# Kernel tuning notes

Hardware: AMD Instinct MI355X
Metric: run time of the kernel (lower is better)

## Reference

```python
import jax, jax.numpy as jnp
import numpy as np
import math

NEIGHBOR_RADIUS = 30.0

def _masked_softmax(logits, mask, axis):
    # mask: bool, True = keep; all-masked rows return zeros
    p = jax.nn.softmax(jnp.where(mask, logits, -1e9), axis=axis) * mask.astype(logits.dtype)
    return p / jnp.clip(jnp.sum(p, axis=axis, keepdims=True), 1e-9, None)

def _forward(agents_state, agents_mask, map_polylines, map_poly_mask,
             map_poly_type, map_tl_status, map_on_route,
             pm_w1, pm_b1, pm_w2, pm_b2, type_emb, tl_emb, route_emb,
             mo_w1, mo_b1, mo_w2, mo_b2,
             ae_w1, ae_b1, ae_w2, ae_b2, ae_w3, ae_b3,
             mr_w1, mr_b1, mr_w2, mr_b2,
             nr_w1, nr_b1, nr_w2, nr_b2,
             to_w1, to_b1, to_w2, to_b2):
    relu = jax.nn.relu
    a_mask = (agents_mask > 0.5).astype(agents_state.dtype)   # (B,N,T)
    a_feat = agents_state[..., :5]
    # ---- map polyline node encoder ----
    h = relu(map_polylines @ pm_w1 + pm_b1)                   # (B,M,L,H)
    h = relu(h @ pm_w2 + pm_b2)
    h = h.max(axis=2)                                         # (B,M,H) max-pool over points
    t_idx = jnp.clip(map_poly_type, 0, type_emb.shape[0] - 1)
    s_idx = jnp.clip(map_tl_status, 0, tl_emb.shape[0] - 1)
    r_idx = jnp.clip(map_on_route, 0, route_emb.shape[0] - 1)
    h = h + type_emb[t_idx] + tl_emb[s_idx] + route_emb[r_idx]
    h = relu(h @ mo_w1 + mo_b1) @ mo_w2 + mo_b2
    map_mask = map_poly_mask > 0.5                            # (B,M) bool
    map_node = h * map_mask[..., None].astype(h.dtype)        # (B,M,D)
    map_center = map_polylines.mean(axis=2)                   # (B,M,2)
    # ---- agent state encoder ----
    a = relu(a_feat @ ae_w1 + ae_b1)
    a = relu(a @ ae_w2 + ae_b2)
    a_emb = (a @ ae_w3 + ae_b3) * a_mask[..., None]           # (B,N,T,D)
    D = a_emb.shape[-1]
    # ---- agent -> map attention ----
    agent_pos = a_feat[..., 0:2]
    rel = map_center[:, None, None, :, :] - agent_pos[:, :, :, None, :]  # (B,N,T,M,2)
    dist = jnp.linalg.norm(rel, axis=-1, keepdims=True)
    rel_feat = jnp.concatenate([rel, dist], axis=-1)          # (B,N,T,M,3)
    rel_score = (relu(rel_feat @ mr_w1 + mr_b1) @ mr_w2 + mr_b2)[..., 0]  # (B,N,T,M)
    dot = jnp.einsum('bntd,bmd->bntm', a_emb, map_node) / math.sqrt(D)
    score_mask = jnp.broadcast_to(map_mask[:, None, None, :], dot.shape)
    attn = _masked_softmax(dot + rel_score, score_mask, axis=-1)
    map_ctx = jnp.einsum('bntm,bmd->bntd', attn, map_node)    # (B,N,T,D)
    # ---- neighbor graph attention ----
    pos = a_feat[..., 0:2]
    vel = a_feat[..., 3:5]
    pos_j = jnp.transpose(pos, (0, 2, 1, 3))                  # (B,T,N,2)
    vel_j = jnp.transpose(vel, (0, 2, 1, 3))
    rel_pos = pos_j[:, None, :, :, :] - pos[:, :, :, None, :] # (B,N,T,N,2) = p_j - p_i
    rel_vel = vel_j[:, None, :, :, :] - vel[:, :, :, None, :]
    dist_ij = jnp.linalg.norm(rel_pos, axis=-1, keepdims=True)
    rel_ij = jnp.concatenate([rel_pos, rel_vel, dist_ij], axis=-1)        # (B,N,T,N,5)
    nbr_score = (relu(rel_ij @ nr_w1 + nr_b1) @ nr_w2 + nr_b2)[..., 0]    # (B,N,T,N)
    am_b = agents_mask > 0.5
    valid_i = am_b[..., None]                                 # (B,N,T,1)
    valid_j = jnp.transpose(am_b, (0, 2, 1))[:, None, :, :]   # (B,1,T,N)
    N = pos.shape[1]
    not_self = ~jnp.eye(N, dtype=bool)[None, :, None, :]      # (1,N,1,N)
    nbr_mask = valid_i & valid_j & (dist_ij[..., 0] <= NEIGHBOR_RADIUS) & not_self
    dot_n = jnp.einsum('bitd,bjtd->bitj', a_emb, a_emb) / math.sqrt(D)
    w_n = _masked_softmax(dot_n + nbr_score, nbr_mask, axis=-1)
    nbr_ctx = jnp.einsum('bitj,bjtd->bitd', w_n, a_emb)       # (B,N,T,D)
    # ---- tau head ----
    tau = jnp.concatenate([a_emb, map_ctx, nbr_ctx], axis=-1)
    tau = relu(tau @ to_w1 + to_b1) @ to_w2 + to_b2
    return tau * a_mask[..., None]

def setup_inputs() -> dict:
    key = jax.random.key(0)
    B, N, T, M, L = 2, 32, 32, 256, 20
    H, D, TAU = 128, 128, 64
    ks = jax.random.split(key, 32)
    def f(i, shp):
        return jax.random.normal(ks[i], shp, jnp.float32) * 0.05
    inp = {}
    inp['agents_state'] = jax.random.normal(ks[0], (B, N, T, 5), jnp.float32) * jnp.array([50., 50., 1., 5., 5.], jnp.float32)
    inp['agents_mask'] = jnp.ones((B, N, T), jnp.float32)
    inp['map_polylines'] = jax.random.normal(ks[1], (B, M, L, 2), jnp.float32) * 50.0
    inp['map_poly_mask'] = jnp.ones((B, M), jnp.float32)
    inp['map_poly_type'] = jax.random.randint(ks[2], (B, M), 0, 4)
    inp['map_tl_status'] = jax.random.randint(ks[3], (B, M), 0, 8)
    inp['map_on_route'] = jax.random.randint(ks[4], (B, M), 0, 2)
    inp['pm_w1'] = f(5, (2, H));  inp['pm_b1'] = jnp.zeros((H,), jnp.float32)
    inp['pm_w2'] = f(6, (H, H)); inp['pm_b2'] = jnp.zeros((H,), jnp.float32)
    inp['type_emb'] = f(7, (4, H)); inp['tl_emb'] = f(8, (8, H)); inp['route_emb'] = f(9, (2, H))
    inp['mo_w1'] = f(10, (H, H)); inp['mo_b1'] = jnp.zeros((H,), jnp.float32)
    inp['mo_w2'] = f(11, (H, D)); inp['mo_b2'] = jnp.zeros((D,), jnp.float32)
    inp['ae_w1'] = f(12, (5, H)); inp['ae_b1'] = jnp.zeros((H,), jnp.float32)
    inp['ae_w2'] = f(13, (H, H)); inp['ae_b2'] = jnp.zeros((H,), jnp.float32)
    inp['ae_w3'] = f(14, (H, D)); inp['ae_b3'] = jnp.zeros((D,), jnp.float32)
    inp['mr_w1'] = f(15, (3, H)); inp['mr_b1'] = jnp.zeros((H,), jnp.float32)
    inp['mr_w2'] = f(16, (H, 1)); inp['mr_b2'] = jnp.zeros((1,), jnp.float32)
    inp['nr_w1'] = f(17, (5, H)); inp['nr_b1'] = jnp.zeros((H,), jnp.float32)
    inp['nr_w2'] = f(18, (H, 1)); inp['nr_b2'] = jnp.zeros((1,), jnp.float32)
    inp['to_w1'] = f(19, (3 * D, H)); inp['to_b1'] = jnp.zeros((H,), jnp.float32)
    inp['to_w2'] = f(20, (H, TAU)); inp['to_b2'] = jnp.zeros((TAU,), jnp.float32)
    return inp

def reference(agents_state, agents_mask, map_polylines, map_poly_mask,
              map_poly_type, map_tl_status, map_on_route,
              pm_w1, pm_b1, pm_w2, pm_b2, type_emb, tl_emb, route_emb,
              mo_w1, mo_b1, mo_w2, mo_b2,
              ae_w1, ae_b1, ae_w2, ae_b2, ae_w3, ae_b3,
              mr_w1, mr_b1, mr_w2, mr_b2,
              nr_w1, nr_b1, nr_w2, nr_b2,
              to_w1, to_b1, to_w2, to_b2):
    return _forward(agents_state, agents_mask, map_polylines, map_poly_mask,
                    map_poly_type, map_tl_status, map_on_route,
                    pm_w1, pm_b1, pm_w2, pm_b2, type_emb, tl_emb, route_emb,
                    mo_w1, mo_b1, mo_w2, mo_b2,
                    ae_w1, ae_b1, ae_w2, ae_b2, ae_w3, ae_b3,
                    mr_w1, mr_b1, mr_w2, mr_b2,
                    nr_w1, nr_b1, nr_w2, nr_b2,
                    to_w1, to_b1, to_w2, to_b2)
```

## Files before the change

kernel.cpp:

```cpp
#include <hip/hip_runtime.h>
#include <hip/hip_bf16.h>

#define Bb 2
#define Nn 32
#define Tt 32
#define Mm 256
#define Ll 20
#define Hh 128
#define Dd 128
#define TAUu 64
#define RSQRT_D 0.08838834764831843f

__global__ __launch_bounds__(256) void k_map(
    const float* __restrict__ poly, const float* __restrict__ pmask,
    const int* __restrict__ ptype, const int* __restrict__ ptl, const int* __restrict__ proute,
    const float* __restrict__ pm_w1, const float* __restrict__ pm_b1,
    const float* __restrict__ pm_w2, const float* __restrict__ pm_b2,
    const float* __restrict__ type_emb, const float* __restrict__ tl_emb, const float* __restrict__ route_emb,
    const float* __restrict__ mo_w1, const float* __restrict__ mo_b1,
    const float* __restrict__ mo_w2, const float* __restrict__ mo_b2,
    float* __restrict__ map_node, float* __restrict__ map_nodeT, float* __restrict__ map_center)
{
    int bm = blockIdx.x;
    int b  = bm >> 8;
    int m  = bm & 255;
    int tid = threadIdx.x;
    int h    = tid & 127;
    int half = tid >> 7;
    __shared__ float pts[Ll*2];
    __shared__ float h1a[Ll][Hh];
    __shared__ float hv[Hh];
    __shared__ float red[Hh];
    if (tid < Ll*2) pts[tid] = poly[bm*Ll*2 + tid];
    __syncthreads();
    float w1x = pm_w1[h];
    float w1y = pm_w1[Hh+h];
    float bb1 = pm_b1[h];
    int l0 = half*10;
    #pragma unroll
    for (int u = 0; u < 10; ++u) {
        int l = l0 + u;
        h1a[l][h] = fmaxf(fmaf(w1x, pts[2*l], fmaf(w1y, pts[2*l+1], bb1)), 0.f);
    }
    __syncthreads();
    float bb2 = pm_b2[h];
    float acc[10];
    #pragma unroll
    for (int u = 0; u < 10; ++u) acc[u] = bb2;
    for (int k = 0; k < Hh; ++k) {
        float w = pm_w2[k*Hh + h];
        #pragma unroll
        for (int u = 0; u < 10; ++u) acc[u] = fmaf(h1a[l0+u][k], w, acc[u]);
    }
    float mx = 0.f;
    #pragma unroll
    for (int u = 0; u < 10; ++u) mx = fmaxf(mx, acc[u]);
    if (half == 1) red[h] = mx;
    __syncthreads();
    if (half == 0) {
        float mm2 = fmaxf(mx, red[h]);
        int ti = min(max(ptype[bm], 0), 3);
        int si = min(max(ptl[bm], 0), 7);
        int ri = min(max(proute[bm], 0), 1);
        hv[h] = mm2 + type_emb[ti*Hh+h] + tl_emb[si*Hh+h] + route_emb[ri*Hh+h];
    }
    __syncthreads();
    float a1 = 0.f;
    for (int k = half*64; k < half*64 + 64; ++k) a1 = fmaf(hv[k], mo_w1[k*Hh+h], a1);
    if (half == 1) red[h] = a1;
    __syncthreads();
    if (half == 0) hv[h] = fmaxf(a1 + red[h] + mo_b1[h], 0.f);
    __syncthreads();
    float a2 = 0.f;
    for (int k = half*64; k < half*64 + 64; ++k) a2 = fmaf(hv[k], mo_w2[k*Dd+h], a2);
    if (half == 1) red[h] = a2;
    __syncthreads();
    if (half == 0) {
        float val = a2 + red[h] + mo_b2[h];
        float mk = (pmask[bm] > 0.5f) ? 1.f : 0.f;
        val *= mk;
        map_node[bm*Dd + h] = val;
        map_nodeT[(b*Dd + h)*Mm + m] = val;
    }
    if (tid == 0) {
        float sx = 0.f, sy = 0.f;
        for (int l = 0; l < Ll; ++l) { sx += pts[2*l]; sy += pts[2*l+1]; }
        map_center[bm*2+0] = sx / (float)Ll;
        map_center[bm*2+1] = sy / (float)Ll;
    }
}

__global__ __launch_bounds__(128) void k_agent(
    const float* __restrict__ astate, const float* __restrict__ amask,
    const float* __restrict__ ae_w1, const float* __restrict__ ae_b1,
    const float* __restrict__ ae_w2, const float* __restrict__ ae_b2,
    const float* __restrict__ ae_w3, const float* __restrict__ ae_b3,
    float* __restrict__ a_emb)
{
    int r0 = blockIdx.x * 4;
    int h  = threadIdx.x;
    __shared__ float f5[4][5];
    __shared__ float a1s[4][Hh];
    if (h < 20) f5[h/5][h%5] = astate[(r0 + h/5)*5 + (h%5)];
    __syncthreads();
    float acc[4];
    float b1v = ae_b1[h];
    #pragma unroll
    for (int r = 0; r < 4; ++r) acc[r] = b1v;
    #pragma unroll
    for (int k = 0; k < 5; ++k) {
        float w = ae_w1[k*Hh + h];
        #pragma unroll
        for (int r = 0; r < 4; ++r) acc[r] = fmaf(f5[r][k], w, acc[r]);
    }
    #pragma unroll
    for (int r = 0; r < 4; ++r) a1s[r][h] = fmaxf(acc[r], 0.f);
    __syncthreads();
    float b2v = ae_b2[h];
    #pragma unroll
    for (int r = 0; r < 4; ++r) acc[r] = b2v;
    for (int k = 0; k < Hh; ++k) {
        float w = ae_w2[k*Hh + h];
        #pragma unroll
        for (int r = 0; r < 4; ++r) acc[r] = fmaf(a1s[r][k], w, acc[r]);
    }
    float v2[4];
    #pragma unroll
    for (int r = 0; r < 4; ++r) v2[r] = fmaxf(acc[r], 0.f);
    __syncthreads();
    #pragma unroll
    for (int r = 0; r < 4; ++r) a1s[r][h] = v2[r];
    __syncthreads();
    float b3v = ae_b3[h];
    #pragma unroll
    for (int r = 0; r < 4; ++r) acc[r] = b3v;
    for (int k = 0; k < Hh; ++k) {
        float w = ae_w3[k*Dd + h];
        #pragma unroll
        for (int r = 0; r < 4; ++r) acc[r] = fmaf(a1s[r][k], w, acc[r]);
    }
    #pragma unroll
    for (int r = 0; r < 4; ++r) {
        float mk = (amask[r0+r] > 0.5f) ? 1.f : 0.f;
        a_emb[(r0+r)*Dd + h] = acc[r] * mk;
    }
}

__global__ __launch_bounds__(256) void k_mapattn(
    const float* __restrict__ astate, const float* __restrict__ pmask,
    const float* __restrict__ a_emb, const float* __restrict__ map_node,
    const float* __restrict__ map_nodeT, const float* __restrict__ map_center,
    const float* __restrict__ mr_w1, const float* __restrict__ mr_b1,
    const float* __restrict__ mr_w2, const float* __restrict__ mr_b2,
    float* __restrict__ map_ctx)
{
    int r0  = blockIdx.x * 4;
    int b   = r0 >> 10;
    int tid = threadIdx.x;
    __shared__ float w1m[3*Hh];
    __shared__ float b1m[Hh];
    __shared__ float w2m[Hh];
    __shared__ float pxy4[4][2];
    __shared__ float ae4[4][Dd];
    __shared__ float lg4[4][Mm];
    __shared__ float redc[4][Dd];
    for (int q = tid; q < 3*Hh; q += 256) w1m[q] = mr_w1[q];
    if (tid < Hh) { b1m[tid] = mr_b1[tid]; w2m[tid] = mr_w2[tid]; }
    for (int q = tid; q < 512; q += 256) ae4[q>>7][q&127] = a_emb[(r0 + (q>>7))*Dd + (q&127)];
    if (tid < 8) pxy4[tid>>1][tid&1] = astate[(r0 + (tid>>1))*5 + (tid&1)];
    float b2c = mr_b2[0];
    __syncthreads();

    {
        int m = tid;
        float cx = map_center[(b*Mm+m)*2+0];
        float cy = map_center[(b*Mm+m)*2+1];
        float rx[4], ry[4], dv[4], sA[4], dt[4];
        #pragma unroll
        for (int r = 0; r < 4; ++r) {
            rx[r] = cx - pxy4[r][0];
            ry[r] = cy - pxy4[r][1];
            dv[r] = sqrtf(rx[r]*rx[r] + ry[r]*ry[r]);
            sA[r] = b2c;
            dt[r] = 0.f;
        }
        for (int hh = 0; hh < Hh; ++hh) {
            float wa = w1m[hh], wb = w1m[Hh+hh], wc = w1m[2*Hh+hh];
            float bbv = b1m[hh], w2v = w2m[hh];
            #pragma unroll
            for (int r = 0; r < 4; ++r) {
                float t1 = fmaxf(fmaf(rx[r], wa, fmaf(ry[r], wb, fmaf(dv[r], wc, bbv))), 0.f);
                sA[r] = fmaf(t1, w2v, sA[r]);
            }
        }
        for (int d = 0; d < Dd; ++d) {
            float v = map_nodeT[(b*Dd + d)*Mm + m];
            #pragma unroll
            for (int r = 0; r < 4; ++r) dt[r] = fmaf(ae4[r][d], v, dt[r]);
        }
        bool mk = pmask[b*Mm+m] > 0.5f;
        #pragma unroll
        for (int r = 0; r < 4; ++r)
            lg4[r][m] = mk ? fmaf(dt[r], RSQRT_D, sA[r]) : -1e30f;
    }
    __syncthreads();

    {
        int w = tid >> 6, lam = tid & 63;
        float x0 = lg4[w][lam], x1 = lg4[w][64+lam], x2 = lg4[w][128+lam], x3 = lg4[w][192+lam];
        float mxv = fmaxf(fmaxf(x0,x1), fmaxf(x2,x3));
        for (int off = 32; off; off >>= 1) mxv = fmaxf(mxv, __shfl_xor(mxv, off));
        float e0 = (x0 > -1e29f) ? expf(x0-mxv) : 0.f;
        float e1 = (x1 > -1e29f) ? expf(x1-mxv) : 0.f;
        float e2 = (x2 > -1e29f) ? expf(x2-mxv) : 0.f;
        float e3 = (x3 > -1e29f) ? expf(x3-mxv) : 0.f;
        float sm = e0+e1+e2+e3;
        for (int off = 32; off; off >>= 1) sm += __shfl_xor(sm, off);
        float inv = 1.f / fmaxf(sm, 1e-9f);
        lg4[w][lam]     = e0*inv;
        lg4[w][64+lam]  = e1*inv;
        lg4[w][128+lam] = e2*inv;
        lg4[w][192+lam] = e3*inv;
    }
    __syncthreads();

    {
        int d = tid & 127, hf = tid >> 7;
        float acc[4] = {0.f, 0.f, 0.f, 0.f};
        for (int mm = 0; mm < 128; ++mm) {
            int m2 = (hf<<7) + mm;
            float v = map_node[(b*Mm+m2)*Dd + d];
            #pragma unroll
            for (int r = 0; r < 4; ++r) acc[r] = fmaf(lg4[r][m2], v, acc[r]);
        }
        if (hf == 1) {
            #pragma unroll
            for (int r = 0; r < 4; ++r) redc[r][d] = acc[r];
        }
        __syncthreads();
        if (hf == 0) {
            #pragma unroll
            for (int r = 0; r < 4; ++r) map_ctx[(r0+r)*Dd + d] = acc[r] + redc[r][d];
        }
    }
}

__global__ __launch_bounds__(256) void k_nbr_out(
    const float* __restrict__ astate, const float* __restrict__ amask,
    const float* __restrict__ a_emb, const float* __restrict__ map_ctx,
    const float* __restrict__ nr_w1, const float* __restrict__ nr_b1,
    const float* __restrict__ nr_w2, const float* __restrict__ nr_b2,
    const float* __restrict__ to_w1, const float* __restrict__ to_b1,
    const float* __restrict__ to_w2, const float* __restrict__ to_b2,
    float* __restrict__ out)
{
    int r0 = blockIdx.x * 4;
    int b  = r0 >> 10;
    int i  = (r0 >> 5) & 31;
    int t0 = r0 & 31;
    int tid = threadIdx.x;
    __shared__ float w1n[5*Hh];
    __shared__ float b1n[Hh];
    __shared__ float w2n[Hh];
    __shared__ float ei4[4][Dd];
    __shared__ float tau[4][3*Dd];
    __shared__ float jdat[4][Nn][5];
    __shared__ float rowdat[4][5];
    __shared__ float lgn[4][Nn];
    __shared__ float g1s[4][Hh];
    __shared__ float redn[4][Dd];

    for (int q = tid; q < 5*Hh; q += 256) w1n[q] = nr_w1[q];
    if (tid < Hh) { b1n[tid] = nr_b1[tid]; w2n[tid] = nr_w2[tid]; }
    for (int q = tid; q < 512; q += 256) {
        int rr = q>>7, d = q&127;
        float v = a_emb[(r0+rr)*Dd + d];
        ei4[rr][d] = v;
        tau[rr][d] = v;
        tau[rr][Dd + d] = map_ctx[(r0+rr)*Dd + d];
    }
    if (tid < 128) {
        int rr = tid >> 5, j = tid & 31;
        int rj = ((b*Nn + j)*Tt + t0 + rr);
        jdat[rr][j][0] = astate[rj*5+0];
        jdat[rr][j][1] = astate[rj*5+1];
        jdat[rr][j][2] = astate[rj*5+3];
        jdat[rr][j][3] = astate[rj*5+4];
        jdat[rr][j][4] = amask[rj];
    }
    if (tid < 4) {
        int ri_ = r0 + tid;
        rowdat[tid][0] = astate[ri_*5+0];
        rowdat[tid][1] = astate[ri_*5+1];
        rowdat[tid][2] = astate[ri_*5+3];
        rowdat[tid][3] = astate[ri_*5+4];
        rowdat[tid][4] = amask[ri_];
    }
    float b2c = nr_b2[0];
    __syncthreads();

    {
        int j = tid >> 3, c = tid & 7;
        float mlp[4], dtn[4], ddv[4];
        #pragma unroll
        for (int r = 0; r < 4; ++r) {
            float rpx = jdat[r][j][0] - rowdat[r][0];
            float rpy = jdat[r][j][1] - rowdat[r][1];
            float rvx = jdat[r][j][2] - rowdat[r][2];
            float rvy = jdat[r][j][3] - rowdat[r][3];
            float dd = sqrtf(rpx*rpx + rpy*rpy);
            int rj = ((b*Nn + j)*Tt + t0 + r);
            const float* ej = a_emb + (size_t)rj*Dd;
            float am = 0.f, ad = 0.f;
            #pragma unroll 4
            for (int u = 0; u < 16; ++u) {
                int hh = (u<<3) + c;
                float t1 = fmaf(rpx, w1n[hh], fmaf(rpy, w1n[Hh+hh],
                           fmaf(rvx, w1n[2*Hh+hh], fmaf(rvy, w1n[3*Hh+hh],
                           fmaf(dd,  w1n[4*Hh+hh], b1n[hh])))));
                t1 = fmaxf(t1, 0.f);
                am = fmaf(t1, w2n[hh], am);
                ad = fmaf(ei4[r][hh], ej[hh], ad);
            }
            am += __shfl_xor(am, 1); ad += __shfl_xor(ad, 1);
            am += __shfl_xor(am, 2); ad += __shfl_xor(ad, 2);
            am += __shfl_xor(am, 4); ad += __shfl_xor(ad, 4);
            mlp[r] = am; dtn[r] = ad; ddv[r] = dd;
        }
        if (c == 0) {
            #pragma unroll
            for (int r = 0; r < 4; ++r) {
                bool vi = rowdat[r][4] > 0.5f;
                bool vj = jdat[r][j][4] > 0.5f;
                bool ok = vi && vj && (ddv[r] <= 30.0f) && (j != i);
                lgn[r][j] = ok ? fmaf(dtn[r], RSQRT_D, b2c + mlp[r]) : -1e30f;
            }
        }
    }
    __syncthreads();

    {
        int w = tid >> 6, lam = tid & 63;
        float x = (lam < Nn) ? lgn[w][lam] : -1e30f;
        float mxv = x;
        for (int off = 32; off; off >>= 1) mxv = fmaxf(mxv, __shfl_xor(mxv, off));
        float e = (x > -1e29f) ? expf(x - mxv) : 0.f;
        float sm = e;
        for (int off = 32; off; off >>= 1) sm += __shfl_xor(sm, off);
        float inv = 1.f / fmaxf(sm, 1e-9f);
        if (lam < Nn) lgn[w][lam] = e * inv;
    }
    __syncthreads();

    {
        int d = tid & 127, hf = tid >> 7;
        float acc[4] = {0.f,0.f,0.f,0.f};
        for (int jj = 0; jj < 16; ++jj) {
            int j2 = (hf<<4) + jj;
            #pragma unroll
            for (int r = 0; r < 4; ++r) {
                float v = a_emb[((size_t)((b*Nn + j2)*Tt + t0 + r))*Dd + d];
                acc[r] = fmaf(lgn[r][j2], v, acc[r]);
            }
        }
        if (hf == 1) {
            #pragma unroll
            for (int r = 0; r < 4; ++r) redn[r][d] = acc[r];
        }
        __syncthreads();
        if (hf == 0) {
            #pragma unroll
            for (int r = 0; r < 4; ++r) tau[r][2*Dd + d] = acc[r] + redn[r][d];
        }
    }
    __syncthreads();

    {
        int h = tid & 127, rp = tid >> 7;
        float accA = 0.f, accB = 0.f;
        for (int k = 0; k < 3*Dd; ++k) {
            float w = to_w1[k*Hh + h];
            accA = fmaf(tau[rp][k],   w, accA);
            accB = fmaf(tau[rp+2][k], w, accB);
        }
        float bv = to_b1[h];
        g1s[rp][h]   = fmaxf(accA + bv, 0.f);
        g1s[rp+2][h] = fmaxf(accB + bv, 0.f);
    }
    __syncthreads();

    {
        int o = tid & 63, row = tid >> 6;
        float acc = to_b2[o];
        for (int hh = 0; hh < Hh; ++hh) acc = fmaf(g1s[row][hh], to_w2[hh*TAUu + o], acc);
        float vi = (rowdat[row][4] > 0.5f) ? 1.f : 0.f;
        out[(r0+row)*TAUu + o] = acc * vi;
    }
}

extern "C" void kernel_launch(void* const* d_in, const int* in_sizes, int n_in,
                              void* d_out, int out_size, void* d_ws, size_t ws_size,
                              hipStream_t stream) {
    const float* agents_state  = (const float*)d_in[0];
    const float* agents_mask   = (const float*)d_in[1];
    const float* map_polylines = (const float*)d_in[2];
    const float* map_poly_mask = (const float*)d_in[3];
    const int*   map_poly_type = (const int*)d_in[4];
    const int*   map_tl_status = (const int*)d_in[5];
    const int*   map_on_route  = (const int*)d_in[6];
    const float* pm_w1 = (const float*)d_in[7];
    const float* pm_b1 = (const float*)d_in[8];
    const float* pm_w2 = (const float*)d_in[9];
    const float* pm_b2 = (const float*)d_in[10];
    const float* type_emb  = (const float*)d_in[11];
    const float* tl_emb    = (const float*)d_in[12];
    const float* route_emb = (const float*)d_in[13];
    const float* mo_w1 = (const float*)d_in[14];
    const float* mo_b1 = (const float*)d_in[15];
    const float* mo_w2 = (const float*)d_in[16];
    const float* mo_b2 = (const float*)d_in[17];
    const float* ae_w1 = (const float*)d_in[18];
    const float* ae_b1 = (const float*)d_in[19];
    const float* ae_w2 = (const float*)d_in[20];
    const float* ae_b2 = (const float*)d_in[21];
    const float* ae_w3 = (const float*)d_in[22];
    const float* ae_b3 = (const float*)d_in[23];
    const float* mr_w1 = (const float*)d_in[24];
    const float* mr_b1 = (const float*)d_in[25];
    const float* mr_w2 = (const float*)d_in[26];
    const float* mr_b2 = (const float*)d_in[27];
    const float* nr_w1 = (const float*)d_in[28];
    const float* nr_b1 = (const float*)d_in[29];
    const float* nr_w2 = (const float*)d_in[30];
    const float* nr_b2 = (const float*)d_in[31];
    const float* to_w1 = (const float*)d_in[32];
    const float* to_b1 = (const float*)d_in[33];
    const float* to_w2 = (const float*)d_in[34];
    const float* to_b2 = (const float*)d_in[35];

    float* ws = (float*)d_ws;
    float* map_node   = ws;
    float* map_nodeT  = ws + 65536;
    float* map_center = ws + 131072;
    float* a_emb      = ws + 132096;
    float* map_ctx    = ws + 394240;

    float* out = (float*)d_out;

    k_map<<<Bb*Mm, 256, 0, stream>>>(map_polylines, map_poly_mask,
        map_poly_type, map_tl_status, map_on_route,
        pm_w1, pm_b1, pm_w2, pm_b2, type_emb, tl_emb, route_emb,
        mo_w1, mo_b1, mo_w2, mo_b2, map_node, map_nodeT, map_center);

    k_agent<<<Bb*Nn*Tt/4, 128, 0, stream>>>(agents_state, agents_mask,
        ae_w1, ae_b1, ae_w2, ae_b2, ae_w3, ae_b3, a_emb);

    k_mapattn<<<Bb*Nn*Tt/4, 256, 0, stream>>>(agents_state, map_poly_mask,
        a_emb, map_node, map_nodeT, map_center, mr_w1, mr_b1, mr_w2, mr_b2, map_ctx);

    k_nbr_out<<<Bb*Nn*Tt/4, 256, 0, stream>>>(agents_state, agents_mask,
        a_emb, map_ctx, nr_w1, nr_b1, nr_w2, nr_b2,
        to_w1, to_b1, to_w2, to_b2, out);
}
```

Before: 202.4 us.

## Fuse map-attention into neighbor/output kernel and use readlane-broadcast matvecs

Merges the map-attention and neighbor/output kernels into one kernel, which drops the map_ctx round trip through global memory and one launch. The MLP matvecs in k_map, k_agent and the output head now broadcast activations across lanes with readlane instead of reading them from shared memory. k_map also drops to 128 threads, with 20 rows per thread held in registers. The cost is much higher register pressure and heavier fully unrolled loops, which may lower occupancy.

```diff
diff --git a/kernel.cpp b/kernel.cpp
--- a/kernel.cpp
+++ b/kernel.cpp
@@ -11,7 +11,11 @@
 #define TAUu 64
 #define RSQRT_D 0.08838834764831843f
 
-__global__ __launch_bounds__(256) void k_map(
+__device__ __forceinline__ float rlane(float v, int l) {
+    return __int_as_float(__builtin_amdgcn_readlane(__float_as_int(v), l));
+}
+
+__global__ __launch_bounds__(128) void k_map(
     const float* __restrict__ poly, const float* __restrict__ pmask,
     const int* __restrict__ ptype, const int* __restrict__ ptl, const int* __restrict__ proute,
     const float* __restrict__ pm_w1, const float* __restrict__ pm_b1,
@@ -22,69 +26,90 @@
     float* __restrict__ map_node, float* __restrict__ map_nodeT, float* __restrict__ map_center)
 {
     int bm = blockIdx.x;
-    int b  = bm >> 8;
-    int m  = bm & 255;
-    int tid = threadIdx.x;
-    int h    = tid & 127;
-    int half = tid >> 7;
-    __shared__ float pts[Ll*2];
-    __shared__ float h1a[Ll][Hh];
-    __shared__ float hv[Hh];
-    __shared__ float red[Hh];
-    if (tid < Ll*2) pts[tid] = poly[bm*Ll*2 + tid];
-    __syncthreads();
-    float w1x = pm_w1[h];
-    float w1y = pm_w1[Hh+h];
-    float bb1 = pm_b1[h];
-    int l0 = half*10;
-    #pragma unroll
-    for (int u = 0; u < 10; ++u) {
-        int l = l0 + u;
-        h1a[l][h] = fmaxf(fmaf(w1x, pts[2*l], fmaf(w1y, pts[2*l+1], bb1)), 0.f);
-    }
-    __syncthreads();
-    float bb2 = pm_b2[h];
-    float acc[10];
-    #pragma unroll
-    for (int u = 0; u < 10; ++u) acc[u] = bb2;
-    for (int k = 0; k < Hh; ++k) {
+    int b  = bm >> 8, m = bm & 255;
+    int h  = threadIdx.x;
+    int lam = h & 63, wv = h >> 6;
+    int obase = ((wv ^ 1) << 6) + lam;
+    __shared__ float xch[Ll][Hh];
+
+    const float* pp = poly + bm * (Ll*2);
+    float w1x = pm_w1[h], w1y = pm_w1[Hh+h], b1v = pm_b1[h];
+    float h1r[Ll];
+    #pragma unroll
+    for (int l = 0; l < Ll; ++l) {
+        float xl = pp[2*l], yl = pp[2*l+1];
+        h1r[l] = fmaxf(fmaf(w1x, xl, fmaf(w1y, yl, b1v)), 0.f);
+    }
+    #pragma unroll
+    for (int l = 0; l < Ll; ++l) xch[l][h] = h1r[l];
+    __syncthreads();
+    float lo[Ll], hi[Ll];
+    #pragma unroll
+    for (int l = 0; l < Ll; ++l) {
+        float o = xch[l][obase];
+        lo[l] = wv ? o : h1r[l];
+        hi[l] = wv ? h1r[l] : o;
+    }
+    float b2v = pm_b2[h];
+    float acc[Ll];
+    #pragma unroll
+    for (int l = 0; l < Ll; ++l) acc[l] = b2v;
+    #pragma unroll
+    for (int k = 0; k < 64; ++k) {
         float w = pm_w2[k*Hh + h];
         #pragma unroll
-        for (int u = 0; u < 10; ++u) acc[u] = fmaf(h1a[l0+u][k], w, acc[u]);
+        for (int l = 0; l < Ll; ++l) acc[l] = fmaf(rlane(lo[l], k), w, acc[l]);
+    }
+    #pragma unroll
+    for (int k = 0; k < 64; ++k) {
+        float w = pm_w2[(64+k)*Hh + h];
+        #pragma unroll
+        for (int l = 0; l < Ll; ++l) acc[l] = fmaf(rlane(hi[l], k), w, acc[l]);
     }
     float mx = 0.f;
     #pragma unroll
-    for (int u = 0; u < 10; ++u) mx = fmaxf(mx, acc[u]);
-    if (half == 1) red[h] = mx;
-    __syncthreads();
-    if (half == 0) {
-        float mm2 = fmaxf(mx, red[h]);
-        int ti = min(max(ptype[bm], 0), 3);
-        int si = min(max(ptl[bm], 0), 7);
-        int ri = min(max(proute[bm], 0), 1);
-        hv[h] = mm2 + type_emb[ti*Hh+h] + tl_emb[si*Hh+h] + route_emb[ri*Hh+h];
-    }
-    __syncthreads();
-    float a1 = 0.f;
-    for (int k = half*64; k < half*64 + 64; ++k) a1 = fmaf(hv[k], mo_w1[k*Hh+h], a1);
-    if (half == 1) red[h] = a1;
-    __syncthreads();
-    if (half == 0) hv[h] = fmaxf(a1 + red[h] + mo_b1[h], 0.f);
-    __syncthreads();
-    float a2 = 0.f;
-    for (int k = half*64; k < half*64 + 64; ++k) a2 = fmaf(hv[k], mo_w2[k*Dd+h], a2);
-    if (half == 1) red[h] = a2;
-    __syncthreads();
-    if (half == 0) {
-        float val = a2 + red[h] + mo_b2[h];
-        float mk = (pmask[bm] > 0.5f) ? 1.f : 0.f;
-        val *= mk;
-        map_node[bm*Dd + h] = val;
-        map_nodeT[(b*Dd + h)*Mm + m] = val;
-    }
-    if (tid == 0) {
+    for (int l = 0; l < Ll; ++l) mx = fmaxf(mx, acc[l]);
+
+    int ti = min(max(ptype[bm], 0), 3);
+    int si = min(max(ptl[bm], 0), 7);
+    int ri = min(max(proute[bm], 0), 1);
+    float hval = mx + type_emb[ti*Hh+h] + tl_emb[si*Hh+h] + route_emb[ri*Hh+h];
+
+    __syncthreads();
+    xch[0][h] = hval;
+    __syncthreads();
+    {
+        float o = xch[0][obase];
+        float l1 = wv ? o : hval, h1 = wv ? hval : o;
+        float a1 = mo_b1[h];
+        #pragma unroll
+        for (int k = 0; k < 64; ++k) a1 = fmaf(rlane(l1, k), mo_w1[k*Hh + h], a1);
+        #pragma unroll
+        for (int k = 0; k < 64; ++k) a1 = fmaf(rlane(h1, k), mo_w1[(64+k)*Hh + h], a1);
+        hval = fmaxf(a1, 0.f);
+    }
+    __syncthreads();
+    xch[0][h] = hval;
+    __syncthreads();
+    float val;
+    {
+        float o = xch[0][obase];
+        float l1 = wv ? o : hval, h1 = wv ? hval : o;
+        float a2 = mo_b2[h];
+        #pragma unroll
+        for (int k = 0; k < 64; ++k) a2 = fmaf(rlane(l1, k), mo_w2[k*Dd + h], a2);
+        #pragma unroll
+        for (int k = 0; k < 64; ++k) a2 = fmaf(rlane(h1, k), mo_w2[(64+k)*Dd + h], a2);
+        val = a2;
+    }
+    float mk = (pmask[bm] > 0.5f) ? 1.f : 0.f;
+    val *= mk;
+    map_node[bm*Dd + h] = val;
+    map_nodeT[(b*Dd + h)*Mm + m] = val;
+    if (h == 0) {
         float sx = 0.f, sy = 0.f;
-        for (int l = 0; l < Ll; ++l) { sx += pts[2*l]; sy += pts[2*l+1]; }
+        #pragma unroll
+        for (int l = 0; l < Ll; ++l) { sx += pp[2*l]; sy += pp[2*l+1]; }
         map_center[bm*2+0] = sx / (float)Ll;
         map_center[bm*2+1] = sy / (float)Ll;
     }
@@ -99,155 +124,88 @@
 {
     int r0 = blockIdx.x * 4;
     int h  = threadIdx.x;
-    __shared__ float f5[4][5];
-    __shared__ float a1s[4][Hh];
-    if (h < 20) f5[h/5][h%5] = astate[(r0 + h/5)*5 + (h%5)];
-    __syncthreads();
-    float acc[4];
+    int lam = h & 63, wv = h >> 6;
+    int obase = ((wv ^ 1) << 6) + lam;
+    __shared__ float xch[4][Hh];
+
+    float w1[5];
+    #pragma unroll
+    for (int k = 0; k < 5; ++k) w1[k] = ae_w1[k*Hh + h];
     float b1v = ae_b1[h];
-    #pragma unroll
-    for (int r = 0; r < 4; ++r) acc[r] = b1v;
-    #pragma unroll
-    for (int k = 0; k < 5; ++k) {
-        float w = ae_w1[k*Hh + h];
-        #pragma unroll
-        for (int r = 0; r < 4; ++r) acc[r] = fmaf(f5[r][k], w, acc[r]);
-    }
-    #pragma unroll
-    for (int r = 0; r < 4; ++r) a1s[r][h] = fmaxf(acc[r], 0.f);
-    __syncthreads();
+    float a1[4];
+    #pragma unroll
+    for (int r = 0; r < 4; ++r) {
+        const float* st = astate + (r0+r)*5;
+        float a = b1v;
+        #pragma unroll
+        for (int k = 0; k < 5; ++k) a = fmaf(w1[k], st[k], a);
+        a1[r] = fmaxf(a, 0.f);
+    }
+    #pragma unroll
+    for (int r = 0; r < 4; ++r) xch[r][h] = a1[r];
+    __syncthreads();
+    float lo[4], hi[4];
+    #pragma unroll
+    for (int r = 0; r < 4; ++r) {
+        float o = xch[r][obase];
+        lo[r] = wv ? o : a1[r];
+        hi[r] = wv ? a1[r] : o;
+    }
     float b2v = ae_b2[h];
-    #pragma unroll
-    for (int r = 0; r < 4; ++r) acc[r] = b2v;
-    for (int k = 0; k < Hh; ++k) {
+    float ac[4] = {b2v, b2v, b2v, b2v};
+    #pragma unroll
+    for (int k = 0; k < 64; ++k) {
         float w = ae_w2[k*Hh + h];
         #pragma unroll
-        for (int r = 0; r < 4; ++r) acc[r] = fmaf(a1s[r][k], w, acc[r]);
-    }
-    float v2[4];
-    #pragma unroll
-    for (int r = 0; r < 4; ++r) v2[r] = fmaxf(acc[r], 0.f);
-    __syncthreads();
-    #pragma unroll
-    for (int r = 0; r < 4; ++r) a1s[r][h] = v2[r];
-    __syncthreads();
+        for (int r = 0; r < 4; ++r) ac[r] = fmaf(rlane(lo[r], k), w, ac[r]);
+    }
+    #pragma unroll
+    for (int k = 0; k < 64; ++k) {
+        float w = ae_w2[(64+k)*Hh + h];
+        #pragma unroll
+        for (int r = 0; r < 4; ++r) ac[r] = fmaf(rlane(hi[r], k), w, ac[r]);
+    }
+    #pragma unroll
+    for (int r = 0; r < 4; ++r) a1[r] = fmaxf(ac[r], 0.f);
+    __syncthreads();
+    #pragma unroll
+    for (int r = 0; r < 4; ++r) xch[r][h] = a1[r];
+    __syncthreads();
+    #pragma unroll
+    for (int r = 0; r < 4; ++r) {
+        float o = xch[r][obase];
+        lo[r] = wv ? o : a1[r];
+        hi[r] = wv ? a1[r] : o;
+    }
     float b3v = ae_b3[h];
     #pragma unroll
-    for (int r = 0; r < 4; ++r) acc[r] = b3v;
-    for (int k = 0; k < Hh; ++k) {
+    for (int r = 0; r < 4; ++r) ac[r] = b3v;
+    #pragma unroll
+    for (int k = 0; k < 64; ++k) {
         float w = ae_w3[k*Dd + h];
         #pragma unroll
-        for (int r = 0; r < 4; ++r) acc[r] = fmaf(a1s[r][k], w, acc[r]);
+        for (int r = 0; r < 4; ++r) ac[r] = fmaf(rlane(lo[r], k), w, ac[r]);
+    }
+    #pragma unroll
+    for (int k = 0; k < 64; ++k) {
+        float w = ae_w3[(64+k)*Dd + h];
+        #pragma unroll
+        for (int r = 0; r < 4; ++r) ac[r] = fmaf(rlane(hi[r], k), w, ac[r]);
     }
     #pragma unroll
     for (int r = 0; r < 4; ++r) {
         float mk = (amask[r0+r] > 0.5f) ? 1.f : 0.f;
-        a_emb[(r0+r)*Dd + h] = acc[r] * mk;
+        a_emb[(r0+r)*Dd + h] = ac[r] * mk;
     }
 }
 
-__global__ __launch_bounds__(256) void k_mapattn(
-    const float* __restrict__ astate, const float* __restrict__ pmask,
+__global__ __launch_bounds__(256) void k_fused(
+    const float* __restrict__ astate, const float* __restrict__ amask,
+    const float* __restrict__ pmask,
     const float* __restrict__ a_emb, const float* __restrict__ map_node,
     const float* __restrict__ map_nodeT, const float* __restrict__ map_center,
     const float* __restrict__ mr_w1, const float* __restrict__ mr_b1,
     const float* __restrict__ mr_w2, const float* __restrict__ mr_b2,
-    float* __restrict__ map_ctx)
-{
-    int r0  = blockIdx.x * 4;
-    int b   = r0 >> 10;
-    int tid = threadIdx.x;
-    __shared__ float w1m[3*Hh];
-    __shared__ float b1m[Hh];
-    __shared__ float w2m[Hh];
-    __shared__ float pxy4[4][2];
-    __shared__ float ae4[4][Dd];
-    __shared__ float lg4[4][Mm];
-    __shared__ float redc[4][Dd];
-    for (int q = tid; q < 3*Hh; q += 256) w1m[q] = mr_w1[q];
-    if (tid < Hh) { b1m[tid] = mr_b1[tid]; w2m[tid] = mr_w2[tid]; }
-    for (int q = tid; q < 512; q += 256) ae4[q>>7][q&127] = a_emb[(r0 + (q>>7))*Dd + (q&127)];
-    if (tid < 8) pxy4[tid>>1][tid&1] = astate[(r0 + (tid>>1))*5 + (tid&1)];
-    float b2c = mr_b2[0];
-    __syncthreads();
-
-    {
-        int m = tid;
-        float cx = map_center[(b*Mm+m)*2+0];
-        float cy = map_center[(b*Mm+m)*2+1];
-        float rx[4], ry[4], dv[4], sA[4], dt[4];
-        #pragma unroll
-        for (int r = 0; r < 4; ++r) {
-            rx[r] = cx - pxy4[r][0];
-            ry[r] = cy - pxy4[r][1];
-            dv[r] = sqrtf(rx[r]*rx[r] + ry[r]*ry[r]);
-            sA[r] = b2c;
-            dt[r] = 0.f;
-        }
-        for (int hh = 0; hh < Hh; ++hh) {
-            float wa = w1m[hh], wb = w1m[Hh+hh], wc = w1m[2*Hh+hh];
-            float bbv = b1m[hh], w2v = w2m[hh];
-            #pragma unroll
-            for (int r = 0; r < 4; ++r) {
-                float t1 = fmaxf(fmaf(rx[r], wa, fmaf(ry[r], wb, fmaf(dv[r], wc, bbv))), 0.f);
-                sA[r] = fmaf(t1, w2v, sA[r]);
-            }
-        }
-        for (int d = 0; d < Dd; ++d) {
-            float v = map_nodeT[(b*Dd + d)*Mm + m];
-            #pragma unroll
-            for (int r = 0; r < 4; ++r) dt[r] = fmaf(ae4[r][d], v, dt[r]);
-        }
-        bool mk = pmask[b*Mm+m] > 0.5f;
-        #pragma unroll
-        for (int r = 0; r < 4; ++r)
-            lg4[r][m] = mk ? fmaf(dt[r], RSQRT_D, sA[r]) : -1e30f;
-    }
-    __syncthreads();
-
-    {
-        int w = tid >> 6, lam = tid & 63;
-        float x0 = lg4[w][lam], x1 = lg4[w][64+lam], x2 = lg4[w][128+lam], x3 = lg4[w][192+lam];
-        float mxv = fmaxf(fmaxf(x0,x1), fmaxf(x2,x3));
-        for (int off = 32; off; off >>= 1) mxv = fmaxf(mxv, __shfl_xor(mxv, off));
-        float e0 = (x0 > -1e29f) ? expf(x0-mxv) : 0.f;
-        float e1 = (x1 > -1e29f) ? expf(x1-mxv) : 0.f;
-        float e2 = (x2 > -1e29f) ? expf(x2-mxv) : 0.f;
-        float e3 = (x3 > -1e29f) ? expf(x3-mxv) : 0.f;
-        float sm = e0+e1+e2+e3;
-        for (int off = 32; off; off >>= 1) sm += __shfl_xor(sm, off);
-        float inv = 1.f / fmaxf(sm, 1e-9f);
-        lg4[w][lam]     = e0*inv;
-        lg4[w][64+lam]  = e1*inv;
-        lg4[w][128+lam] = e2*inv;
-        lg4[w][192+lam] = e3*inv;
-    }
-    __syncthreads();
-
-    {
-        int d = tid & 127, hf = tid >> 7;
-        float acc[4] = {0.f, 0.f, 0.f, 0.f};
-        for (int mm = 0; mm < 128; ++mm) {
-            int m2 = (hf<<7) + mm;
-            float v = map_node[(b*Mm+m2)*Dd + d];
-            #pragma unroll
-            for (int r = 0; r < 4; ++r) acc[r] = fmaf(lg4[r][m2], v, acc[r]);
-        }
-        if (hf == 1) {
-            #pragma unroll
-            for (int r = 0; r < 4; ++r) redc[r][d] = acc[r];
-        }
-        __syncthreads();
-        if (hf == 0) {
-            #pragma unroll
-            for (int r = 0; r < 4; ++r) map_ctx[(r0+r)*Dd + d] = acc[r] + redc[r][d];
-        }
-    }
-}
-
-__global__ __launch_bounds__(256) void k_nbr_out(
-    const float* __restrict__ astate, const float* __restrict__ amask,
-    const float* __restrict__ a_emb, const float* __restrict__ map_ctx,
     const float* __restrict__ nr_w1, const float* __restrict__ nr_b1,
     const float* __restrict__ nr_w2, const float* __restrict__ nr_b2,
     const float* __restrict__ to_w1, const float* __restrict__ to_b1,
@@ -259,142 +217,241 @@
     int i  = (r0 >> 5) & 31;
     int t0 = r0 & 31;
     int tid = threadIdx.x;
-    __shared__ float w1n[5*Hh];
-    __shared__ float b1n[Hh];
-    __shared__ float w2n[Hh];
-    __shared__ float ei4[4][Dd];
+    int lam = tid & 63, wv = tid >> 6;
+
     __shared__ float tau[4][3*Dd];
-    __shared__ float jdat[4][Nn][5];
-    __shared__ float rowdat[4][5];
+    __shared__ float lg4[4][Mm];
+    __shared__ float p4[Mm][4];
+    __shared__ float ctxp[4][512];
+    __shared__ float w1n_s[5*Hh];
+    __shared__ float b1n_s[Hh];
+    __shared__ float w2n_s[Hh];
+    __shared__ float jd[4][Nn][5];
     __shared__ float lgn[4][Nn];
+    __shared__ float p4n[Nn][4];
     __shared__ float g1s[4][Hh];
-    __shared__ float redn[4][Dd];
-
-    for (int q = tid; q < 5*Hh; q += 256) w1n[q] = nr_w1[q];
-    if (tid < Hh) { b1n[tid] = nr_b1[tid]; w2n[tid] = nr_w2[tid]; }
-    for (int q = tid; q < 512; q += 256) {
-        int rr = q>>7, d = q&127;
-        float v = a_emb[(r0+rr)*Dd + d];
-        ei4[rr][d] = v;
-        tau[rr][d] = v;
-        tau[rr][Dd + d] = map_ctx[(r0+rr)*Dd + d];
-    }
+
+    for (int q = tid; q < 512; q += 256) tau[q>>7][q&127] = a_emb[(r0 + (q>>7))*Dd + (q&127)];
+    for (int q = tid; q < 5*Hh; q += 256) w1n_s[q] = nr_w1[q];
+    if (tid < Hh) { b1n_s[tid] = nr_b1[tid]; w2n_s[tid] = nr_w2[tid]; }
     if (tid < 128) {
         int rr = tid >> 5, j = tid & 31;
-        int rj = ((b*Nn + j)*Tt + t0 + rr);
-        jdat[rr][j][0] = astate[rj*5+0];
-        jdat[rr][j][1] = astate[rj*5+1];
-        jdat[rr][j][2] = astate[rj*5+3];
-        jdat[rr][j][3] = astate[rj*5+4];
-        jdat[rr][j][4] = amask[rj];
-    }
-    if (tid < 4) {
-        int ri_ = r0 + tid;
-        rowdat[tid][0] = astate[ri_*5+0];
-        rowdat[tid][1] = astate[ri_*5+1];
-        rowdat[tid][2] = astate[ri_*5+3];
-        rowdat[tid][3] = astate[ri_*5+4];
-        rowdat[tid][4] = amask[ri_];
-    }
-    float b2c = nr_b2[0];
+        int rj = (b*Nn + j)*Tt + t0 + rr;
+        jd[rr][j][0] = astate[rj*5+0];
+        jd[rr][j][1] = astate[rj*5+1];
+        jd[rr][j][2] = astate[rj*5+3];
+        jd[rr][j][3] = astate[rj*5+4];
+        jd[rr][j][4] = amask[rj];
+    }
+    __syncthreads();
+
+    {
+        int m = tid;
+        float cx = map_center[(b*Mm+m)*2+0];
+        float cy = map_center[(b*Mm+m)*2+1];
+        float rx[4], ry[4], dv[4], sA[4], dt[4];
+        float b2c = mr_b2[0];
+        #pragma unroll
+        for (int r = 0; r < 4; ++r) {
+            float px = astate[(r0+r)*5+0];
+            float py = astate[(r0+r)*5+1];
+            rx[r] = cx - px; ry[r] = cy - py;
+            dv[r] = sqrtf(rx[r]*rx[r] + ry[r]*ry[r]);
+            sA[r] = b2c; dt[r] = 0.f;
+        }
+        #pragma unroll 4
+        for (int k = 0; k < Hh; ++k) {
+            float wa = mr_w1[k], wb = mr_w1[Hh+k], wc = mr_w1[2*Hh+k];
+            float bb = mr_b1[k], w2 = mr_w2[k];
+            #pragma unroll
+            for (int r = 0; r < 4; ++r) {
+                float t1 = fmaf(rx[r], wa, fmaf(ry[r], wb, fmaf(dv[r], wc, bb)));
+                t1 = fmaxf(t1, 0.f);
+                sA[r] = fmaf(t1, w2, sA[r]);
+            }
+        }
+        #pragma unroll 4
+        for (int d = 0; d < Dd; ++d) {
+            float v = map_nodeT[(b*Dd + d)*Mm + m];
+            #pragma unroll
+            for (int r = 0; r < 4; ++r)
+                dt[r] = fmaf(v, a_emb[(r0+r)*Dd + d], dt[r]);
+        }
+        bool mk = pmask[b*Mm+m] > 0.5f;
+        #pragma unroll
+        for (int r = 0; r < 4; ++r)
+            lg4[r][m] = mk ? fmaf(dt[r], RSQRT_D, sA[r]) : -1e30f;
+    }
+    __syncthreads();
+
+    {
+        float x0 = lg4[wv][lam], x1 = lg4[wv][64+lam], x2 = lg4[wv][128+lam], x3 = lg4[wv][192+lam];
+        float mxv = fmaxf(fmaxf(x0,x1), fmaxf(x2,x3));
+        for (int off = 32; off; off >>= 1) mxv = fmaxf(mxv, __shfl_xor(mxv, off));
+        float e0 = (x0 > -1e29f) ? expf(x0-mxv) : 0.f;
+        float e1 = (x1 > -1e29f) ? expf(x1-mxv) : 0.f;
+        float e2 = (x2 > -1e29f) ? expf(x2-mxv) : 0.f;
+        float e3 = (x3 > -1e29f) ? expf(x3-mxv) : 0.f;
+        float sm = e0+e1+e2+e3;
+        for (int off = 32; off; off >>= 1) sm += __shfl_xor(sm, off);
+        float inv = 1.f / fmaxf(sm, 1e-9f);
+        p4[lam][wv]     = e0*inv;
+        p4[64+lam][wv]  = e1*inv;
+        p4[128+lam][wv] = e2*inv;
+        p4[192+lam][wv] = e3*inv;
+    }
+    __syncthreads();
+
+    {
+        int m0 = wv * 64;
+        float4 pv = *(const float4*)&p4[m0 + lam][0];
+        float pr0 = pv.x, pr1 = pv.y, pr2 = pv.z, pr3 = pv.w;
+        float a00=0.f,a01=0.f,a10=0.f,a11=0.f,a20=0.f,a21=0.f,a30=0.f,a31=0.f;
+        #pragma unroll
+        for (int mm = 0; mm < 64; ++mm) {
+            const float* np = map_node + (b*Mm + m0 + mm)*Dd;
+            float v0 = np[lam], v1 = np[64+lam];
+            float s0 = rlane(pr0, mm), s1 = rlane(pr1, mm), s2 = rlane(pr2, mm), s3 = rlane(pr3, mm);
+            a00 = fmaf(s0, v0, a00); a01 = fmaf(s0, v1, a01);
+            a10 = fmaf(s1, v0, a10); a11 = fmaf(s1, v1, a11);
+            a20 = fmaf(s2, v0, a20); a21 = fmaf(s2, v1, a21);
+            a30 = fmaf(s3, v0, a30); a31 = fmaf(s3, v1, a31);
+        }
+        ctxp[wv][0*Dd + lam] = a00; ctxp[wv][0*Dd + 64+lam] = a01;
+        ctxp[wv][1*Dd + lam] = a10; ctxp[wv][1*Dd + 64+lam] = a11;
+        ctxp[wv][2*Dd + lam] = a20; ctxp[wv][2*Dd + 64+lam] = a21;
+        ctxp[wv][3*Dd + lam] = a30; ctxp[wv][3*Dd + 64+lam] = a31;
+    }
+    __syncthreads();
+    for (int q = tid; q < 512; q += 256) {
+        float s = ctxp[0][q] + ctxp[1][q] + ctxp[2][q] + ctxp[3][q];
+        tau[q>>7][Dd + (q&127)] = s;
+    }
     __syncthreads();
 
     {
         int j = tid >> 3, c = tid & 7;
-        float mlp[4], dtn[4], ddv[4];
+        float b2c = nr_b2[0];
+        float rpx[4], rpy[4], rvx[4], rvy[4], dd[4], am[4], ad[4];
         #pragma unroll
         for (int r = 0; r < 4; ++r) {
-            float rpx = jdat[r][j][0] - rowdat[r][0];
-            float rpy = jdat[r][j][1] - rowdat[r][1];
-            float rvx = jdat[r][j][2] - rowdat[r][2];
-            float rvy = jdat[r][j][3] - rowdat[r][3];
-            float dd = sqrtf(rpx*rpx + rpy*rpy);
-            int rj = ((b*Nn + j)*Tt + t0 + r);
-            const float* ej = a_emb + (size_t)rj*Dd;
-            float am = 0.f, ad = 0.f;
-            #pragma unroll 4
-            for (int u = 0; u < 16; ++u) {
-                int hh = (u<<3) + c;
-                float t1 = fmaf(rpx, w1n[hh], fmaf(rpy, w1n[Hh+hh],
-                           fmaf(rvx, w1n[2*Hh+hh], fmaf(rvy, w1n[3*Hh+hh],
-                           fmaf(dd,  w1n[4*Hh+hh], b1n[hh])))));
+            float pxi = astate[(r0+r)*5+0], pyi = astate[(r0+r)*5+1];
+            float vxi = astate[(r0+r)*5+3], vyi = astate[(r0+r)*5+4];
+            rpx[r] = jd[r][j][0] - pxi; rpy[r] = jd[r][j][1] - pyi;
+            rvx[r] = jd[r][j][2] - vxi; rvy[r] = jd[r][j][3] - vyi;
+            dd[r]  = sqrtf(rpx[r]*rpx[r] + rpy[r]*rpy[r]);
+            am[r] = 0.f; ad[r] = 0.f;
+        }
+        #pragma unroll
+        for (int u = 0; u < 16; ++u) {
+            int hh = (u<<3) + c;
+            float wA = w1n_s[hh], wB = w1n_s[Hh+hh], wC = w1n_s[2*Hh+hh];
+            float wD = w1n_s[3*Hh+hh], wE = w1n_s[4*Hh+hh];
+            float bb = b1n_s[hh], w2 = w2n_s[hh];
+            #pragma unroll
+            for (int r = 0; r < 4; ++r) {
+                float t1 = fmaf(rpx[r], wA, fmaf(rpy[r], wB, fmaf(rvx[r], wC,
+                           fmaf(rvy[r], wD, fmaf(dd[r], wE, bb)))));
                 t1 = fmaxf(t1, 0.f);
-                am = fmaf(t1, w2n[hh], am);
-                ad = fmaf(ei4[r][hh], ej[hh], ad);
+                am[r] = fmaf(t1, w2, am[r]);
+                float ejv = a_emb[((size_t)((b*Nn + j)*Tt + t0 + r))*Dd + hh];
+                ad[r] = fmaf(tau[r][hh], ejv, ad[r]);
             }
-            am += __shfl_xor(am, 1); ad += __shfl_xor(ad, 1);
-            am += __shfl_xor(am, 2); ad += __shfl_xor(ad, 2);
-            am += __shfl_xor(am, 4); ad += __shfl_xor(ad, 4);
-            mlp[r] = am; dtn[r] = ad; ddv[r] = dd;
+        }
+        #pragma unroll
+        for (int r = 0; r < 4; ++r) {
+            am[r] += __shfl_xor(am[r], 1); ad[r] += __shfl_xor(ad[r], 1);
+            am[r] += __shfl_xor(am[r], 2); ad[r] += __shfl_xor(ad[r], 2);
+            am[r] += __shfl_xor(am[r], 4); ad[r] += __shfl_xor(ad[r], 4);
         }
         if (c == 0) {
             #pragma unroll
             for (int r = 0; r < 4; ++r) {
-                bool vi = rowdat[r][4] > 0.5f;
-                bool vj = jdat[r][j][4] > 0.5f;
-                bool ok = vi && vj && (ddv[r] <= 30.0f) && (j != i);
-                lgn[r][j] = ok ? fmaf(dtn[r], RSQRT_D, b2c + mlp[r]) : -1e30f;
+                bool vi = amask[r0+r] > 0.5f;
+                bool vj = jd[r][j][4] > 0.5f;
+                bool ok = vi && vj && (dd[r] <= 30.0f) && (j != i);
+                lgn[r][j] = ok ? fmaf(ad[r], RSQRT_D, b2c + am[r]) : -1e30f;
             }
         }
     }
     __syncthreads();
 
     {
-        int w = tid >> 6, lam = tid & 63;
-        float x = (lam < Nn) ? lgn[w][lam] : -1e30f;
+        float x = (lam < Nn) ? lgn[wv][lam] : -1e30f;
         float mxv = x;
         for (int off = 32; off; off >>= 1) mxv = fmaxf(mxv, __shfl_xor(mxv, off));
         float e = (x > -1e29f) ? expf(x - mxv) : 0.f;
         float sm = e;
         for (int off = 32; off; off >>= 1) sm += __shfl_xor(sm, off);
         float inv = 1.f / fmaxf(sm, 1e-9f);
-        if (lam < Nn) lgn[w][lam] = e * inv;
+        if (lam < Nn) p4n[lam][wv] = e * inv;
     }
     __syncthreads();
 
     {
         int d = tid & 127, hf = tid >> 7;
-        float acc[4] = {0.f,0.f,0.f,0.f};
+        float ac[4] = {0.f,0.f,0.f,0.f};
+        #pragma unroll
         for (int jj = 0; jj < 16; ++jj) {
             int j2 = (hf<<4) + jj;
-            #pragma unroll
-            for (int r = 0; r < 4; ++r) {
-                float v = a_emb[((size_t)((b*Nn + j2)*Tt + t0 + r))*Dd + d];
-                acc[r] = fmaf(lgn[r][j2], v, acc[r]);
-            }
+            float4 pv = *(const float4*)&p4n[j2][0];
+            size_t base = (size_t)((b*Nn + j2)*Tt + t0);
+            float v0 = a_emb[(base+0)*Dd + d];
+            float v1 = a_emb[(base+1)*Dd + d];
+            float v2 = a_emb[(base+2)*Dd + d];
+            float v3 = a_emb[(base+3)*Dd + d];
+            ac[0] = fmaf(pv.x, v0, ac[0]);
+            ac[1] = fmaf(pv.y, v1, ac[1]);
+            ac[2] = fmaf(pv.z, v2, ac[2]);
+            ac[3] = fmaf(pv.w, v3, ac[3]);
         }
         if (hf == 1) {
             #pragma unroll
-            for (int r = 0; r < 4; ++r) redn[r][d] = acc[r];
+            for (int r = 0; r < 4; ++r) ctxp[0][r*Dd + d] = ac[r];
         }
         __syncthreads();
         if (hf == 0) {
             #pragma unroll
-            for (int r = 0; r < 4; ++r) tau[r][2*Dd + d] = acc[r] + redn[r][d];
+            for (int r = 0; r < 4; ++r) tau[r][2*Dd + d] = ac[r] + ctxp[0][r*Dd + d];
         }
     }
     __syncthreads();
 
     {
         int h = tid & 127, rp = tid >> 7;
-        float accA = 0.f, accB = 0.f;
-        for (int k = 0; k < 3*Dd; ++k) {
-            float w = to_w1[k*Hh + h];
-            accA = fmaf(tau[rp][k],   w, accA);
-            accB = fmaf(tau[rp+2][k], w, accB);
+        float ta[6], tb[6];
+        #pragma unroll
+        for (int c = 0; c < 6; ++c) {
+            ta[c] = tau[rp][c*64 + lam];
+            tb[c] = tau[rp+2][c*64 + lam];
+        }
+        float acc0 = 0.f, acc1 = 0.f;
+        #pragma unroll
+        for (int c = 0; c < 6; ++c) {
+            #pragma unroll
+            for (int kk = 0; kk < 64; ++kk) {
+                float w = to_w1[(c*64+kk)*Hh + h];
+                acc0 = fmaf(rlane(ta[c], kk), w, acc0);
+                acc1 = fmaf(rlane(tb[c], kk), w, acc1);
+            }
         }
         float bv = to_b1[h];
-        g1s[rp][h]   = fmaxf(accA + bv, 0.f);
-        g1s[rp+2][h] = fmaxf(accB + bv, 0.f);
-    }
-    __syncthreads();
-
-    {
-        int o = tid & 63, row = tid >> 6;
-        float acc = to_b2[o];
-        for (int hh = 0; hh < Hh; ++hh) acc = fmaf(g1s[row][hh], to_w2[hh*TAUu + o], acc);
-        float vi = (rowdat[row][4] > 0.5f) ? 1.f : 0.f;
-        out[(r0+row)*TAUu + o] = acc * vi;
+        g1s[rp][h]   = fmaxf(acc0 + bv, 0.f);
+        g1s[rp+2][h] = fmaxf(acc1 + bv, 0.f);
+    }
+    __syncthreads();
+
+    {
+        float ga = g1s[wv][lam], gb = g1s[wv][64+lam];
+        float acc = to_b2[lam];
+        #pragma unroll
+        for (int kk = 0; kk < 64; ++kk)
+            acc = fmaf(rlane(ga, kk), to_w2[kk*TAUu + lam], acc);
+        #pragma unroll
+        for (int kk = 0; kk < 64; ++kk)
+            acc = fmaf(rlane(gb, kk), to_w2[(64+kk)*TAUu + lam], acc);
+        float mk = (amask[r0+wv] > 0.5f) ? 1.f : 0.f;
+        out[(r0+wv)*TAUu + lam] = acc * mk;
     }
 }
 
@@ -443,11 +500,10 @@
     float* map_nodeT  = ws + 65536;
     float* map_center = ws + 131072;
     float* a_emb      = ws + 132096;
-    float* map_ctx    = ws + 394240;
 
     float* out = (float*)d_out;
 
-    k_map<<<Bb*Mm, 256, 0, stream>>>(map_polylines, map_poly_mask,
+    k_map<<<Bb*Mm, 128, 0, stream>>>(map_polylines, map_poly_mask,
         map_poly_type, map_tl_status, map_on_route,
         pm_w1, pm_b1, pm_w2, pm_b2, type_emb, tl_emb, route_emb,
         mo_w1, mo_b1, mo_w2, mo_b2, map_node, map_nodeT, map_center);
@@ -455,10 +511,9 @@
     k_agent<<<Bb*Nn*Tt/4, 128, 0, stream>>>(agents_state, agents_mask,
         ae_w1, ae_b1, ae_w2, ae_b2, ae_w3, ae_b3, a_emb);
 
-    k_mapattn<<<Bb*Nn*Tt/4, 256, 0, stream>>>(agents_state, map_poly_mask,
-        a_emb, map_node, map_nodeT, map_center, mr_w1, mr_b1, mr_w2, mr_b2, map_ctx);
-
-    k_nbr_out<<<Bb*Nn*Tt/4, 256, 0, stream>>>(agents_state, agents_mask,
-        a_emb, map_ctx, nr_w1, nr_b1, nr_w2, nr_b2,
+    k_fused<<<Bb*Nn*Tt/4, 256, 0, stream>>>(agents_state, agents_mask,
+        map_poly_mask, a_emb, map_node, map_nodeT, map_center,
+        mr_w1, mr_b1, mr_w2, mr_b2,
+        nr_w1, nr_b1, nr_w2, nr_b2,
         to_w1, to_b1, to_w2, to_b2, out);
 }
```

New measurement: 210.1 us. +3.8%, slower.
